# Optimization experiments

Measured on AMD Instinct MI355X. Metric: run time of the kernel, lower is better.

Reference implementation:

```python
import jax, jax.numpy as jnp
import numpy as np
from jax import lax

V = 100000       # vocab_size / num_words
E = 300          # embedding_size (== num_units, required by compare stage)
M = 300          # num_units / mem_dim
NC = 3           # num_classes
L = 128          # leaves per tree -> N = 2L-1 nodes
N = 2 * L - 1


def build_tree(num_leaves):
    # balanced binary tree, postorder node numbering (children before parent)
    left, right = [], []
    def rec(lo, hi):
        if hi - lo == 1:
            left.append(-1); right.append(-1)
            return len(left) - 1
        mid = (lo + hi) // 2
        l = rec(lo, mid)
        r = rec(mid, hi)
        left.append(l); right.append(r)
        return len(left) - 1
    rec(0, num_leaves)
    return np.asarray(left, np.int32), np.asarray(right, np.int32)


def setup_inputs() -> dict:
    key = jax.random.key(0)
    ks = jax.random.split(key, 20)
    l1, r1 = build_tree(L)
    l2, r2 = build_tree(L)
    s = 0.1  # param scale (stands in for orthogonal init)
    inp = {
        "sent1": jax.random.randint(ks[0], (N,), 0, V),
        "sent2": jax.random.randint(ks[1], (N,), 0, V),
        "left1": jnp.asarray(l1), "right1": jnp.asarray(r1),
        "left2": jnp.asarray(l2), "right2": jnp.asarray(r2),
        "emb": jax.random.normal(ks[2], (V, E), jnp.float32),
        # composer x-projections, gate order: [cx, ix, fx, ox]
        "Wx_i": jax.random.normal(ks[3], (4, M, E), jnp.float32) * s,
        "bx_i": jnp.zeros((4, M), jnp.float32),
        # composer h-projections, gate order: [u, i, lf, rf, o]
        "Wl_i": jax.random.normal(ks[4], (5, M, M), jnp.float32) * s,
        "Wr_i": jax.random.normal(ks[5], (5, M, M), jnp.float32) * s,
        "Wx_c": jax.random.normal(ks[6], (4, M, M), jnp.float32) * s,
        "bx_c": jnp.zeros((4, M), jnp.float32),
        "Wl_c": jax.random.normal(ks[7], (5, M, M), jnp.float32) * s,
        "Wr_c": jax.random.normal(ks[8], (5, M, M), jnp.float32) * s,
        "Wc": jax.random.normal(ks[9], (M, 4 * M), jnp.float32) * 0.01,
        "bc": jnp.zeros((M,), jnp.float32),
        "Wa1": jax.random.normal(ks[10], (M, 4 * M), jnp.float32) * 0.01,
        "ba1": jnp.zeros((M,), jnp.float32),
        "Wa2": jax.random.normal(ks[11], (NC, M), jnp.float32) * 0.01,
        "ba2": jnp.zeros((NC,), jnp.float32),
    }
    return inp


def tree_lstm(xg, left, right, Wl, Wr):
    # xg: [N, 4, M] precomputed x-gate terms (cx, ix, fx, ox)
    # Wl/Wr: [5, M, M] hidden-state gate weights (u, i, lf, rf, o)
    n, _, m = xg.shape
    zero = jnp.zeros((m,), xg.dtype)

    def step(carry, t):
        C, H = carry
        i, l, r = t
        lc = jnp.where(l >= 0, C[jnp.maximum(l, 0)], zero)
        lh = jnp.where(l >= 0, H[jnp.maximum(l, 0)], zero)
        rc = jnp.where(r >= 0, C[jnp.maximum(r, 0)], zero)
        rh = jnp.where(r >= 0, H[jnp.maximum(r, 0)], zero)
        gl = jnp.einsum('gmd,d->gm', Wl, lh)  # [5, M]
        gr = jnp.einsum('gmd,d->gm', Wr, rh)
        x = xg[i]  # [4, M]
        u  = jnp.tanh(x[0] + gl[0] + gr[0])
        ig = jax.nn.sigmoid(x[1] + gl[1] + gr[1])
        lf = jax.nn.sigmoid(x[2] + gl[2] + gr[2])  # fx shared for both forgets (as in source)
        rf = jax.nn.sigmoid(x[2] + gl[3] + gr[3])
        c = ig * u + lf * lc + rf * rc
        o = jax.nn.sigmoid(x[3] + gl[4] + gr[4])
        h = o * jnp.tanh(c)
        return (C.at[i].set(c), H.at[i].set(h)), None

    init = (jnp.zeros((n, m), xg.dtype), jnp.zeros((n, m), xg.dtype))
    (_, H), _ = lax.scan(step, init, (jnp.arange(n), left, right))
    return H  # [N, M] all node hidden states in postorder


def reference(sent1, sent2, left1, right1, left2, right2, emb,
              Wx_i, bx_i, Wl_i, Wr_i, Wx_c, bx_c, Wl_c, Wr_c,
              Wc, bc, Wa1, ba1, Wa2, ba2):
    pad = emb.shape[0] - 1  # num_words - 1

    def encode(sent, left, right):
        # leaves embed their token; internal nodes embed PAD (PAD=True path)
        tok = jnp.where(left < 0, sent, pad)
        x = emb[tok]                                        # [N, E]
        xg = jnp.einsum('nd,gmd->ngm', x, Wx_i) + bx_i      # [N, 4, M]
        return tree_lstm(xg, left, right, Wl_i, Wr_i)

    s1 = encode(sent1, left1, right1)  # [N1, M]
    s2 = encode(sent2, left2, right2)  # [N2, M]

    raw = s1 @ s2.T                                         # [N1, N2]
    beta = jax.nn.softmax(raw, axis=1) @ s2                 # aligned to s1
    alpha = jax.nn.softmax(raw.T, axis=1) @ s1              # aligned to s2

    def compare(s, a, left, right):
        feat = jnp.concatenate([s, a, s - a, s * a], axis=-1)  # [N, 4M]
        h = jax.nn.relu(feat @ Wc.T + bc)                      # [N, M]
        xg = jnp.einsum('nd,gmd->ngm', h, Wx_c) + bx_c
        return tree_lstm(xg, left, right, Wl_c, Wr_c)

    v1 = compare(s1, beta, left1, right1)
    v2 = compare(s2, alpha, left2, right2)

    agg = jnp.concatenate([v1.mean(0), v1.max(0), v2.mean(0), v2.max(0)])  # [4M]
    hidden = jax.nn.relu(agg @ Wa1.T + ba1)
    logits = hidden @ Wa2.T + ba2
    return logits[None, :]  # [1, num_classes]
```

## Files before the change

kernel.cpp:

```cpp
#include <hip/hip_runtime.h>
#include <math.h>

#define NN 255
#define MM 300
#define TC 510
#define NBLK 300
#define CHUNK 16
#define HTLD 512

__device__ __forceinline__ float sigm(float x) { return 1.0f / (1.0f + expf(-x)); }

__device__ __forceinline__ float aload(const float* p) {
  return __hip_atomic_load(p, __ATOMIC_RELAXED, __HIP_MEMORY_SCOPE_AGENT);
}
__device__ __forceinline__ void astore(float* p, float v) {
  __hip_atomic_store(p, v, __ATOMIC_RELAXED, __HIP_MEMORY_SCOPE_AGENT);
}

__device__ __forceinline__ void leaf_gate(const float* __restrict__ xgp, int m, float& c, float& h) {
  float x0 = xgp[m], x1 = xgp[300 + m], x3 = xgp[900 + m];
  float u  = tanhf(x0);
  float ig = sigm(x1);
  c = ig * u;
  h = sigm(x3) * tanhf(c);
}

__device__ __forceinline__ void gsync(unsigned* flags, unsigned phase) {
  asm volatile("s_waitcnt vmcnt(0)" ::: "memory");
  __syncthreads();
  unsigned* gate = flags + NBLK;
  if (blockIdx.x == 0) {
    if (threadIdx.x < 64) {
      for (;;) {
        unsigned mn = phase;
        for (int i = 1 + (int)threadIdx.x; i < NBLK; i += 64)
          mn = min(mn, __hip_atomic_load(&flags[i], __ATOMIC_RELAXED, __HIP_MEMORY_SCOPE_AGENT));
        if (__all(mn >= phase)) break;
        __builtin_amdgcn_s_sleep(2);
      }
      if (threadIdx.x == 0)
        __hip_atomic_store(gate, phase, __ATOMIC_RELAXED, __HIP_MEMORY_SCOPE_AGENT);
    }
  } else {
    if (threadIdx.x == 0) {
      __hip_atomic_store(&flags[blockIdx.x], phase, __ATOMIC_RELAXED, __HIP_MEMORY_SCOPE_AGENT);
      while (__hip_atomic_load(gate, __ATOMIC_RELAXED, __HIP_MEMORY_SCOPE_AGENT) < phase)
        __builtin_amdgcn_s_sleep(2);
    }
  }
  __syncthreads();
}

__global__ __launch_bounds__(512) void k_setup(const int* __restrict__ l1, const int* __restrict__ r1,
                                               const int* __restrict__ l2, const int* __restrict__ r2,
                                               int4* __restrict__ lists2, int* __restrict__ cnt)
{
  __shared__ int lv[TC];
  __shared__ int cs[16];
  int t = threadIdx.x;
  if (t < TC) lv[t] = 0;
  if (t < 16) cs[t] = 0;
  __syncthreads();
  for (int it = 0; it < 12; ++it) {
    int nv = 0;
    if (t < TC) {
      int tr = t >= NN;
      int i  = t - tr * NN;
      const int* L = tr ? l2 : l1;
      const int* R = tr ? r2 : r1;
      int l = L[i], r = R[i];
      nv = (l < 0) ? 0 : 1 + max(lv[tr * NN + l], lv[tr * NN + r]);
    }
    __syncthreads();
    if (t < TC) lv[t] = nv;
    __syncthreads();
  }
  if (t < TC) {
    int tr = t >= NN;
    int i  = t - tr * NN;
    int v  = min(lv[t], 15);
    int pos = atomicAdd(&cs[v], 1);
    int l = (tr ? l2 : l1)[i], r = (tr ? r2 : r1)[i];
    lists2[v * 256 + pos] = make_int4(tr * NN + i, tr * NN + max(l, 0), tr * NN + max(r, 0), 0);
  }
  __syncthreads();
  if (t < 16) cnt[t] = cs[t];
}

__global__ __launch_bounds__(256, 2) void k_tree(
    const int* __restrict__ l1, const int* __restrict__ l2,
    const float* __restrict__ Wl, const float* __restrict__ Wr,
    const float* __restrict__ xg,
    float* __restrict__ H, float* __restrict__ C, float* __restrict__ HT,
    const int4* __restrict__ lists2, const int* __restrict__ cnt,
    unsigned* __restrict__ bar)
{
  __shared__ float Hs[CHUNK][2][320];
  __shared__ float Cs[CHUNK][4][2];
  __shared__ float Xs[CHUNK][4][4];
  __shared__ int4 nfo[288];
  __shared__ int lvoff[9];

  const int tid  = threadIdx.x;
  const int lane = tid & 63;
  const int team = tid >> 6;
  const int mblk = blockIdx.x % 75;
  const int grp  = blockIdx.x / 75;
  const int m    = mblk * 4 + team;

  float wl[5][5], wr[5][5];
  #pragma unroll
  for (int g = 0; g < 5; ++g) {
    #pragma unroll
    for (int j = 0; j < 5; ++j) {
      int d = j * 64 + lane;
      size_t o = ((size_t)g * 300 + m) * 300 + d;
      wl[g][j] = (d < 300) ? Wl[o] : 0.f;
      wr[g][j] = (d < 300) ? Wr[o] : 0.f;
    }
  }

  if (tid == 0) { int o = 0; for (int lv = 1; lv <= 7; ++lv) { lvoff[lv] = o; o += cnt[lv]; } }
  __syncthreads();
  for (int lv = 1; lv <= 7; ++lv)
    for (int i = tid; i < cnt[lv]; i += 256)
      nfo[lvoff[lv] + i] = lists2[lv * 256 + i];

  for (int e = blockIdx.x * 256 + tid; e < TC * 300; e += 256 * NBLK) {
    int gi = e / 300;
    int mm = e - gi * 300;
    int tr = gi >= NN;
    int node = gi - tr * NN;
    if ((tr ? l2 : l1)[node] < 0) {
      float c, h;
      leaf_gate(xg + (size_t)gi * 1200, mm, c, h);
      astore(&C[(size_t)gi * 300 + mm], c);
      astore(&H[(size_t)gi * 300 + mm], h);
      astore(&HT[(size_t)mm * HTLD + gi], h);
    }
  }
  gsync(bar, 1);

  for (int lv = 1; lv <= 7; ++lv) {
    int nodes = cnt[lv];
    int npg = (nodes + 3) >> 2;
    int n0 = grp * npg;
    int n1 = min(nodes, n0 + npg);
    for (int nb = n0; nb < n1; nb += CHUNK) {
      int nch = min(CHUNK, n1 - nb);
      int base = lvoff[lv] + nb;
      __syncthreads();

      #pragma unroll
      for (int p = 0; p < 2; ++p) {
        int niA = team + p * 8;
        int niB = niA + 4;
        bool vA = niA < nch, vB = niB < nch;
        int4 na = vA ? nfo[base + niA] : make_int4(0, 0, 0, 0);
        int4 nb4 = vB ? nfo[base + niB] : make_int4(0, 0, 0, 0);
        float bA0, bA1, bA2, bA3, bA4, bA5, bA6, bA7, bA8, bA9;
        float bB0, bB1, bB2, bB3, bB4, bB5, bB6, bB7, bB8, bB9;
        #define LD(side_ptr, d, ok) ((ok) ? aload(&H[(size_t)(side_ptr) * 300 + (d)]) : 0.f)
        {
          int d0 = lane, d1 = 64 + lane, d2 = 128 + lane, d3 = 192 + lane, d4 = 256 + lane;
          bool i4 = d4 < 300;
          bA0 = LD(na.y, d0, vA); bA1 = LD(na.y, d1, vA); bA2 = LD(na.y, d2, vA);
          bA3 = LD(na.y, d3, vA); bA4 = LD(na.y, d4, vA && i4);
          bA5 = LD(na.z, d0, vA); bA6 = LD(na.z, d1, vA); bA7 = LD(na.z, d2, vA);
          bA8 = LD(na.z, d3, vA); bA9 = LD(na.z, d4, vA && i4);
          bB0 = LD(nb4.y, d0, vB); bB1 = LD(nb4.y, d1, vB); bB2 = LD(nb4.y, d2, vB);
          bB3 = LD(nb4.y, d3, vB); bB4 = LD(nb4.y, d4, vB && i4);
          bB5 = LD(nb4.z, d0, vB); bB6 = LD(nb4.z, d1, vB); bB7 = LD(nb4.z, d2, vB);
          bB8 = LD(nb4.z, d3, vB); bB9 = LD(nb4.z, d4, vB && i4);
          if (vA) {
            Hs[niA][0][d0] = bA0; Hs[niA][0][d1] = bA1; Hs[niA][0][d2] = bA2;
            Hs[niA][0][d3] = bA3; Hs[niA][0][d4] = bA4;
            Hs[niA][1][d0] = bA5; Hs[niA][1][d1] = bA6; Hs[niA][1][d2] = bA7;
            Hs[niA][1][d3] = bA8; Hs[niA][1][d4] = bA9;
          }
          if (vB) {
            Hs[niB][0][d0] = bB0; Hs[niB][0][d1] = bB1; Hs[niB][0][d2] = bB2;
            Hs[niB][0][d3] = bB3; Hs[niB][0][d4] = bB4;
            Hs[niB][1][d0] = bB5; Hs[niB][1][d1] = bB6; Hs[niB][1][d2] = bB7;
            Hs[niB][1][d3] = bB8; Hs[niB][1][d4] = bB9;
          }
        }
        #undef LD
      }
      if (tid < 128) {
        int ni = tid >> 3, tm = (tid >> 1) & 3, side = tid & 1;
        if (ni < nch) {
          int4 nn = nfo[base + ni];
          int child = side ? nn.z : nn.y;
          Cs[ni][tm][side] = aload(&C[(size_t)child * 300 + mblk * 4 + tm]);
        }
      }
      {
        int ni = tid >> 4, tm = (tid >> 2) & 3, g = tid & 3;
        if (ni < nch) {
          int4 nn = nfo[base + ni];
          Xs[ni][tm][g] = xg[(size_t)nn.x * 1200 + g * 300 + mblk * 4 + tm];
        }
      }
      __syncthreads();

      #pragma unroll 2
      for (int ni = 0; ni < nch; ++ni) {
        float p0 = 0.f, p1 = 0.f, p2 = 0.f, p3 = 0.f, p4 = 0.f;
        #pragma unroll
        for (int j = 0; j < 5; ++j) {
          float hl = Hs[ni][0][j * 64 + lane];
          float hr = Hs[ni][1][j * 64 + lane];
          p0 += wl[0][j] * hl + wr[0][j] * hr;
          p1 += wl[1][j] * hl + wr[1][j] * hr;
          p2 += wl[2][j] * hl + wr[2][j] * hr;
          p3 += wl[3][j] * hl + wr[3][j] * hr;
          p4 += wl[4][j] * hl + wr[4][j] * hr;
        }
        #pragma unroll
        for (int off = 32; off; off >>= 1) {
          p0 += __shfl_xor(p0, off);
          p1 += __shfl_xor(p1, off);
          p2 += __shfl_xor(p2, off);
          p3 += __shfl_xor(p3, off);
          p4 += __shfl_xor(p4, off);
        }
        if (lane == 0) {
          int4 nn = nfo[base + ni];
          int gi = nn.x;
          float lc = Cs[ni][team][0], rc = Cs[ni][team][1];
          float u  = tanhf(Xs[ni][team][0] + p0);
          float ig = sigm (Xs[ni][team][1] + p1);
          float lf = sigm (Xs[ni][team][2] + p2);
          float rf = sigm (Xs[ni][team][2] + p3);
          float o  = sigm (Xs[ni][team][3] + p4);
          float cc = ig * u + lf * lc + rf * rc;
          float hv = o * tanhf(cc);
          astore(&C[(size_t)gi * 300 + m], cc);
          astore(&H[(size_t)gi * 300 + m], hv);
          astore(&HT[(size_t)m * HTLD + gi], hv);
        }
      }
    }
    if (lv < 7) gsync(bar, 1 + lv);
  }
}

__global__ __launch_bounds__(256) void k_xg(const int* __restrict__ sent1, const int* __restrict__ sent2,
                                            const int* __restrict__ l1, const int* __restrict__ l2,
                                            const float* __restrict__ emb, int pad,
                                            const float* __restrict__ W, const float* __restrict__ bias,
                                            const float* __restrict__ hsrc, float* __restrict__ out)
{
  __shared__ float Z[8][300];
  int tx = threadIdx.x, ty = threadIdx.y;
  int t = ty * 64 + tx;
  int colbase = blockIdx.y * 8;
  for (int c = 0; c < 8; ++c) {
    int gcol = colbase + c;
    if (gcol < TC) {
      if (hsrc) {
        for (int k = t; k < 300; k += 256) Z[c][k] = hsrc[(size_t)gcol * 300 + k];
      } else {
        int tr = gcol >= NN;
        int node = gcol - tr * NN;
        const int* L = tr ? l2 : l1;
        const int* S = tr ? sent2 : sent1;
        int tok = (L[node] < 0) ? S[node] : pad;
        const float* e = emb + (size_t)tok * 300;
        for (int k = t; k < 300; k += 256) Z[c][k] = e[k];
      }
    } else {
      for (int k = t; k < 300; k += 256) Z[c][k] = 0.f;
    }
  }
  __syncthreads();
  int r = blockIdx.x * 64 + tx;
  if (r < 1200) {
    float a0 = 0.f, a1 = 0.f;
    const float* wp = W + (size_t)r * 300;
    for (int k = 0; k < 300; k += 4) {
      float4 wv = *(const float4*)(wp + k);
      float4 z0 = *(const float4*)(&Z[ty][k]);
      float4 z1 = *(const float4*)(&Z[ty + 4][k]);
      a0 += wv.x*z0.x + wv.y*z0.y + wv.z*z0.z + wv.w*z0.w;
      a1 += wv.x*z1.x + wv.y*z1.y + wv.z*z1.z + wv.w*z1.w;
    }
    float b = bias[r];
    int g0 = colbase + ty, g1 = colbase + ty + 4;
    if (g0 < TC) out[(size_t)g0 * 1200 + r] = a0 + b;
    if (g1 < TC) out[(size_t)g1 * 1200 + r] = a1 + b;
  }
}

__global__ __launch_bounds__(256) void k_attn(const float* __restrict__ H, const float* __restrict__ HT,
                                              float* __restrict__ ab)
{
  __shared__ float q[300];
  __shared__ float pr[NN];
  __shared__ float red[256];
  int b = blockIdx.x, t = threadIdx.x;
  int dir = b >= NN;
  int i = b - dir * NN;
  const float* Ss = H + (dir ? NN * 300 : 0);
  const float* So = H + (dir ? 0 : NN * 300);
  int oppb = dir ? 0 : NN;
  for (int k = t; k < 300; k += 256) q[k] = Ss[(size_t)i * 300 + k];
  __syncthreads();
  float v = -1e30f;
  if (t < NN) {
    float a = 0.f;
    const float* hp = HT + oppb + t;
    #pragma unroll 4
    for (int k = 0; k < 300; ++k) a += q[k] * hp[(size_t)k * HTLD];
    pr[t] = a;
    v = a;
  }
  red[t] = v;
  __syncthreads();
  for (int s = 128; s > 0; s >>= 1) { if (t < s) red[t] = fmaxf(red[t], red[t + s]); __syncthreads(); }
  float mx = red[0];
  __syncthreads();
  float e = 0.f;
  if (t < NN) { e = expf(pr[t] - mx); pr[t] = e; }
  red[t] = e;
  __syncthreads();
  for (int s = 128; s > 0; s >>= 1) { if (t < s) red[t] += red[t + s]; __syncthreads(); }
  float inv = 1.0f / red[0];
  __syncthreads();
  for (int m = t; m < 300; m += 256) {
    float a = 0.f;
    for (int j = 0; j < NN; ++j) a += pr[j] * So[(size_t)j * 300 + m];
    ab[(size_t)b * 300 + m] = a * inv;
  }
}

__global__ __launch_bounds__(256) void k_hcmp(const float* __restrict__ Henc, const float* __restrict__ ab,
                                              const float* __restrict__ Wc, const float* __restrict__ bc,
                                              float* __restrict__ hc)
{
  __shared__ float Z[8][1200];
  int tx = threadIdx.x, ty = threadIdx.y;
  int t = ty * 64 + tx;
  int colbase = blockIdx.y * 8;
  for (int c = 0; c < 8; ++c) {
    int gcol = colbase + c;
    if (gcol < TC) {
      const float* sp = Henc + (size_t)gcol * 300;
      const float* ap = ab + (size_t)gcol * 300;
      for (int k = t; k < 1200; k += 256) {
        int sel = k >= 900 ? 3 : (k >= 600 ? 2 : (k >= 300 ? 1 : 0));
        int kk = k - sel * 300;
        float s = sp[kk], a = ap[kk];
        Z[c][k] = sel == 0 ? s : sel == 1 ? a : sel == 2 ? (s - a) : (s * a);
      }
    } else {
      for (int k = t; k < 1200; k += 256) Z[c][k] = 0.f;
    }
  }
  __syncthreads();
  int r = blockIdx.x * 64 + tx;
  if (r < 300) {
    float a0 = 0.f, a1 = 0.f;
    const float* wp = Wc + (size_t)r * 1200;
    for (int k = 0; k < 1200; k += 4) {
      float4 wv = *(const float4*)(wp + k);
      float4 z0 = *(const float4*)(&Z[ty][k]);
      float4 z1 = *(const float4*)(&Z[ty + 4][k]);
      a0 += wv.x*z0.x + wv.y*z0.y + wv.z*z0.z + wv.w*z0.w;
      a1 += wv.x*z1.x + wv.y*z1.y + wv.z*z1.z + wv.w*z1.w;
    }
    float b = bc[r];
    int g0 = colbase + ty, g1 = colbase + ty + 4;
    if (g0 < TC) hc[(size_t)g0 * 300 + r] = fmaxf(a0 + b, 0.f);
    if (g1 < TC) hc[(size_t)g1 * 300 + r] = fmaxf(a1 + b, 0.f);
  }
}

__global__ __launch_bounds__(512) void k_head(const float* __restrict__ HTc,
                                              const float* __restrict__ Wa1, const float* __restrict__ ba1,
                                              const float* __restrict__ Wa2, const float* __restrict__ ba2,
                                              float* __restrict__ out)
{
  __shared__ float a_s[1200];
  __shared__ float hid[300];
  int t = threadIdx.x;
  for (int idx = t; idx < 600; idx += 512) {
    int tr = idx >= 300;
    int m = idx - tr * 300;
    const float* p = HTc + (size_t)m * HTLD + tr * NN;
    float s = 0.f, mx = -1e30f;
    for (int n = 0; n < NN; ++n) { float v = p[n]; s += v; mx = fmaxf(mx, v); }
    a_s[tr * 600 + m] = s / 255.0f;
    a_s[tr * 600 + 300 + m] = mx;
  }
  __syncthreads();
  for (int h = t; h < 300; h += 512) {
    float acc = ba1[h];
    const float* wp = Wa1 + (size_t)h * 1200;
    for (int k = 0; k < 1200; k += 4) {
      float4 wv = *(const float4*)(wp + k);
      float4 av = *(const float4*)(&a_s[k]);
      acc += wv.x*av.x + wv.y*av.y + wv.z*av.z + wv.w*av.w;
    }
    hid[h] = fmaxf(acc, 0.f);
  }
  __syncthreads();
  if (t < 192) {
    int c = t >> 6, lane = t & 63;
    float a = 0.f;
    for (int k = lane; k < 300; k += 64) a += Wa2[c * 300 + k] * hid[k];
    for (int off = 32; off > 0; off >>= 1) a += __shfl_down(a, off);
    if (lane == 0) out[c] = a + ba2[c];
  }
}

extern "C" void kernel_launch(void* const* d_in, const int* in_sizes, int n_in,
                              void* d_out, int out_size, void* d_ws, size_t ws_size,
                              hipStream_t stream)
{
  const int*   sent1 = (const int*)d_in[0];
  const int*   sent2 = (const int*)d_in[1];
  const int*   l1    = (const int*)d_in[2];
  const int*   r1    = (const int*)d_in[3];
  const int*   l2    = (const int*)d_in[4];
  const int*   r2    = (const int*)d_in[5];
  const float* emb   = (const float*)d_in[6];
  const float* Wx_i  = (const float*)d_in[7];
  const float* bx_i  = (const float*)d_in[8];
  const float* Wl_i  = (const float*)d_in[9];
  const float* Wr_i  = (const float*)d_in[10];
  const float* Wx_c  = (const float*)d_in[11];
  const float* bx_c  = (const float*)d_in[12];
  const float* Wl_c  = (const float*)d_in[13];
  const float* Wr_c  = (const float*)d_in[14];
  const float* Wc    = (const float*)d_in[15];
  const float* bc    = (const float*)d_in[16];
  const float* Wa1   = (const float*)d_in[17];
  const float* ba1   = (const float*)d_in[18];
  const float* Wa2   = (const float*)d_in[19];
  const float* ba2   = (const float*)d_in[20];
  int V = in_sizes[6] / 300;
  int pad = V - 1;

  char* w = (char*)d_ws;
  unsigned* bar1 = (unsigned*)w;
  unsigned* bar2 = (unsigned*)(w + 2048);
  int* cnt     = (int*)(w + 4096);
  int4* lists2 = (int4*)(w + 4160);
  float* xg   = (float*)(w + 4160 + 65536);
  float* Henc = xg + 612000;
  float* Hcmp = Henc + 153000;
  float* C    = Hcmp + 153000;
  float* ab   = C + 153000;
  float* hc   = ab + 153000;
  float* HTe  = hc + 153000;
  float* HTc  = HTe + 153600;

  hipMemsetAsync((void*)bar1, 0, 4096, stream);
  k_setup<<<1, 512, 0, stream>>>(l1, r1, l2, r2, lists2, cnt);

  dim3 blk(64, 4);

  k_xg<<<dim3(19, 64), blk, 0, stream>>>(sent1, sent2, l1, l2, emb, pad, Wx_i, bx_i, nullptr, xg);
  {
    void* args[] = {(void*)&l1, (void*)&l2,
                    (void*)&Wl_i, (void*)&Wr_i, (void*)&xg,
                    (void*)&Henc, (void*)&C, (void*)&HTe,
                    (void*)&lists2, (void*)&cnt, (void*)&bar1};
    hipLaunchCooperativeKernel((void*)k_tree, dim3(NBLK), dim3(256), args, 0, stream);
  }

  k_attn<<<TC, 256, 0, stream>>>(Henc, HTe, ab);

  k_hcmp<<<dim3(5, 64), blk, 0, stream>>>(Henc, ab, Wc, bc, hc);
  k_xg<<<dim3(19, 64), blk, 0, stream>>>(sent1, sent2, l1, l2, emb, pad, Wx_c, bx_c, hc, xg);
  {
    void* args[] = {(void*)&l1, (void*)&l2,
                    (void*)&Wl_c, (void*)&Wr_c, (void*)&xg,
                    (void*)&Hcmp, (void*)&C, (void*)&HTc,
                    (void*)&lists2, (void*)&cnt, (void*)&bar2};
    hipLaunchCooperativeKernel((void*)k_tree, dim3(NBLK), dim3(256), args, 0, stream);
  }

  k_head<<<1, 512, 0, stream>>>(HTc, Wa1, ba1, Wa2, ba2, (float*)d_out);
}
```

Measured before the change: 503.8 us.

## Double tree-LSTM cooperative grid to 600 blocks and use fence-based barrier

New measurement: 796.8 us. 58.2% more time.

```diff
diff --git a/kernel.cpp b/kernel.cpp
--- a/kernel.cpp
+++ b/kernel.cpp
@@ -2,53 +2,47 @@
 #include <math.h>
 
 #define NN 255
-#define MM 300
 #define TC 510
-#define NBLK 300
-#define CHUNK 16
 #define HTLD 512
 
-__device__ __forceinline__ float sigm(float x) { return 1.0f / (1.0f + expf(-x)); }
-
-__device__ __forceinline__ float aload(const float* p) {
-  return __hip_atomic_load(p, __ATOMIC_RELAXED, __HIP_MEMORY_SCOPE_AGENT);
-}
-__device__ __forceinline__ void astore(float* p, float v) {
-  __hip_atomic_store(p, v, __ATOMIC_RELAXED, __HIP_MEMORY_SCOPE_AGENT);
-}
-
-__device__ __forceinline__ void leaf_gate(const float* __restrict__ xgp, int m, float& c, float& h) {
-  float x0 = xgp[m], x1 = xgp[300 + m], x3 = xgp[900 + m];
-  float u  = tanhf(x0);
-  float ig = sigm(x1);
+typedef unsigned int uint32;
+
+__device__ __forceinline__ float sigm(float x){ return 1.f/(1.f+expf(-x)); }
+
+__device__ __forceinline__ uint32 aloadu(const uint32* p){ return __hip_atomic_load(p, __ATOMIC_RELAXED, __HIP_MEMORY_SCOPE_AGENT); }
+__device__ __forceinline__ void astoreu(uint32* p, uint32 v){ __hip_atomic_store(p, v, __ATOMIC_RELAXED, __HIP_MEMORY_SCOPE_AGENT); }
+
+__device__ __forceinline__ void leaf_gate(const float* __restrict__ xgp, int m, float& c, float& h){
+  float x0 = xgp[m], x1 = xgp[300+m], x3 = xgp[900+m];
+  float u = tanhf(x0), ig = sigm(x1);
   c = ig * u;
   h = sigm(x3) * tanhf(c);
 }
 
-__device__ __forceinline__ void gsync(unsigned* flags, unsigned phase) {
-  asm volatile("s_waitcnt vmcnt(0)" ::: "memory");
-  __syncthreads();
-  unsigned* gate = flags + NBLK;
-  if (blockIdx.x == 0) {
-    if (threadIdx.x < 64) {
-      for (;;) {
-        unsigned mn = phase;
-        for (int i = 1 + (int)threadIdx.x; i < NBLK; i += 64)
-          mn = min(mn, __hip_atomic_load(&flags[i], __ATOMIC_RELAXED, __HIP_MEMORY_SCOPE_AGENT));
+template<int NB>
+__device__ __forceinline__ void gsyncf(uint32* flags, uint32 phase){
+  __builtin_amdgcn_fence(__ATOMIC_RELEASE, "agent");
+  __syncthreads();
+  uint32* gate = flags + NB;
+  if (blockIdx.x == 0){
+    if (threadIdx.x < 64){
+      for(;;){
+        uint32 mn = phase;
+        for (int i = 1 + (int)threadIdx.x; i < NB; i += 64)
+          mn = min(mn, aloadu(&flags[i]));
         if (__all(mn >= phase)) break;
         __builtin_amdgcn_s_sleep(2);
       }
-      if (threadIdx.x == 0)
-        __hip_atomic_store(gate, phase, __ATOMIC_RELAXED, __HIP_MEMORY_SCOPE_AGENT);
+      if (threadIdx.x == 0) astoreu(gate, phase);
     }
   } else {
-    if (threadIdx.x == 0) {
-      __hip_atomic_store(&flags[blockIdx.x], phase, __ATOMIC_RELAXED, __HIP_MEMORY_SCOPE_AGENT);
-      while (__hip_atomic_load(gate, __ATOMIC_RELAXED, __HIP_MEMORY_SCOPE_AGENT) < phase)
-        __builtin_amdgcn_s_sleep(2);
-    }
-  }
-  __syncthreads();
+    if (threadIdx.x == 0){
+      astoreu(&flags[blockIdx.x], phase);
+      while (aloadu(gate) < phase) __builtin_amdgcn_s_sleep(2);
+    }
+  }
+  __syncthreads();
+  __builtin_amdgcn_fence(__ATOMIC_ACQUIRE, "agent");
 }
 
 __global__ __launch_bounds__(512) void k_setup(const int* __restrict__ l1, const int* __restrict__ r1,
@@ -61,11 +55,10 @@
   if (t < TC) lv[t] = 0;
   if (t < 16) cs[t] = 0;
   __syncthreads();
-  for (int it = 0; it < 12; ++it) {
+  for (int it = 0; it < 12; ++it){
     int nv = 0;
-    if (t < TC) {
-      int tr = t >= NN;
-      int i  = t - tr * NN;
+    if (t < TC){
+      int tr = t >= NN, i = t - tr * NN;
       const int* L = tr ? l2 : l1;
       const int* R = tr ? r2 : r1;
       int l = L[i], r = R[i];
@@ -75,10 +68,9 @@
     if (t < TC) lv[t] = nv;
     __syncthreads();
   }
-  if (t < TC) {
-    int tr = t >= NN;
-    int i  = t - tr * NN;
-    int v  = min(lv[t], 15);
+  if (t < TC){
+    int tr = t >= NN, i = t - tr * NN;
+    int v = min(lv[t], 15);
     int pos = atomicAdd(&cs[v], 1);
     int l = (tr ? l2 : l1)[i], r = (tr ? r2 : r1)[i];
     lists2[v * 256 + pos] = make_int4(tr * NN + i, tr * NN + max(l, 0), tr * NN + max(r, 0), 0);
@@ -87,128 +79,107 @@
   if (t < 16) cnt[t] = cs[t];
 }
 
-__global__ __launch_bounds__(256, 2) void k_tree(
+template<int NB, int NG>
+__global__ __launch_bounds__(256, 3) void k_tree(
     const int* __restrict__ l1, const int* __restrict__ l2,
     const float* __restrict__ Wl, const float* __restrict__ Wr,
     const float* __restrict__ xg,
     float* __restrict__ H, float* __restrict__ C, float* __restrict__ HT,
     const int4* __restrict__ lists2, const int* __restrict__ cnt,
-    unsigned* __restrict__ bar)
-{
-  __shared__ float Hs[CHUNK][2][320];
-  __shared__ float Cs[CHUNK][4][2];
-  __shared__ float Xs[CHUNK][4][4];
+    uint32* __restrict__ bar)
+{
+  __shared__ float Hs[16][2][320];
+  __shared__ float Cs[16][4][2];
+  __shared__ float Xs[16][4][4];
   __shared__ int4 nfo[288];
   __shared__ int lvoff[9];
 
-  const int tid  = threadIdx.x;
-  const int lane = tid & 63;
-  const int team = tid >> 6;
-  const int mblk = blockIdx.x % 75;
-  const int grp  = blockIdx.x / 75;
-  const int m    = mblk * 4 + team;
+  const int tid = threadIdx.x;
+  const int lane = tid & 63, team = tid >> 6;
+  const int mblk = blockIdx.x % 75, grp = blockIdx.x / 75;
+  const int m = mblk * 4 + team;
 
   float wl[5][5], wr[5][5];
   #pragma unroll
-  for (int g = 0; g < 5; ++g) {
+  for (int g = 0; g < 5; ++g)
     #pragma unroll
-    for (int j = 0; j < 5; ++j) {
+    for (int j = 0; j < 5; ++j){
       int d = j * 64 + lane;
       size_t o = ((size_t)g * 300 + m) * 300 + d;
       wl[g][j] = (d < 300) ? Wl[o] : 0.f;
       wr[g][j] = (d < 300) ? Wr[o] : 0.f;
     }
-  }
-
-  if (tid == 0) { int o = 0; for (int lv = 1; lv <= 7; ++lv) { lvoff[lv] = o; o += cnt[lv]; } }
+
+  if (tid == 0){ int o = 0; for (int lv = 1; lv <= 7; ++lv){ lvoff[lv] = o; o += cnt[lv]; } }
   __syncthreads();
   for (int lv = 1; lv <= 7; ++lv)
     for (int i = tid; i < cnt[lv]; i += 256)
       nfo[lvoff[lv] + i] = lists2[lv * 256 + i];
 
-  for (int e = blockIdx.x * 256 + tid; e < TC * 300; e += 256 * NBLK) {
-    int gi = e / 300;
-    int mm = e - gi * 300;
-    int tr = gi >= NN;
-    int node = gi - tr * NN;
-    if ((tr ? l2 : l1)[node] < 0) {
-      float c, h;
-      leaf_gate(xg + (size_t)gi * 1200, mm, c, h);
-      astore(&C[(size_t)gi * 300 + mm], c);
-      astore(&H[(size_t)gi * 300 + mm], h);
-      astore(&HT[(size_t)mm * HTLD + gi], h);
-    }
-  }
-  gsync(bar, 1);
-
-  for (int lv = 1; lv <= 7; ++lv) {
+  for (int e = blockIdx.x * 256 + tid; e < TC * 300; e += 256 * NB){
+    int gi = e / 300, mm = e - gi * 300;
+    int tr = gi >= NN, node = gi - tr * NN;
+    if ((tr ? l2 : l1)[node] < 0){
+      float c, h; leaf_gate(xg + (size_t)gi * 1200, mm, c, h);
+      C[(size_t)gi * 300 + mm] = c;
+      H[(size_t)gi * 300 + mm] = h;
+      HT[(size_t)mm * HTLD + gi] = h;
+    }
+  }
+  gsyncf<NB>(bar, 1);
+
+  for (int lv = 1; lv <= 7; ++lv){
     int nodes = cnt[lv];
-    int npg = (nodes + 3) >> 2;
-    int n0 = grp * npg;
-    int n1 = min(nodes, n0 + npg);
-    for (int nb = n0; nb < n1; nb += CHUNK) {
-      int nch = min(CHUNK, n1 - nb);
-      int base = lvoff[lv] + nb;
+    int npg = (nodes + NG - 1) / NG;
+    int n0 = grp * npg, n1 = min(nodes, n0 + npg);
+    for (int nb0 = n0; nb0 < n1; nb0 += 16){
+      int nch = min(16, n1 - nb0);
+      int base = lvoff[lv] + nb0;
       __syncthreads();
-
       #pragma unroll
-      for (int p = 0; p < 2; ++p) {
-        int niA = team + p * 8;
-        int niB = niA + 4;
+      for (int p = 0; p < 2; ++p){
+        int niA = team + p * 8, niB = niA + 4;
         bool vA = niA < nch, vB = niB < nch;
         int4 na = vA ? nfo[base + niA] : make_int4(0, 0, 0, 0);
         int4 nb4 = vB ? nfo[base + niB] : make_int4(0, 0, 0, 0);
-        float bA0, bA1, bA2, bA3, bA4, bA5, bA6, bA7, bA8, bA9;
-        float bB0, bB1, bB2, bB3, bB4, bB5, bB6, bB7, bB8, bB9;
-        #define LD(side_ptr, d, ok) ((ok) ? aload(&H[(size_t)(side_ptr) * 300 + (d)]) : 0.f)
-        {
-          int d0 = lane, d1 = 64 + lane, d2 = 128 + lane, d3 = 192 + lane, d4 = 256 + lane;
-          bool i4 = d4 < 300;
-          bA0 = LD(na.y, d0, vA); bA1 = LD(na.y, d1, vA); bA2 = LD(na.y, d2, vA);
-          bA3 = LD(na.y, d3, vA); bA4 = LD(na.y, d4, vA && i4);
-          bA5 = LD(na.z, d0, vA); bA6 = LD(na.z, d1, vA); bA7 = LD(na.z, d2, vA);
-          bA8 = LD(na.z, d3, vA); bA9 = LD(na.z, d4, vA && i4);
-          bB0 = LD(nb4.y, d0, vB); bB1 = LD(nb4.y, d1, vB); bB2 = LD(nb4.y, d2, vB);
-          bB3 = LD(nb4.y, d3, vB); bB4 = LD(nb4.y, d4, vB && i4);
-          bB5 = LD(nb4.z, d0, vB); bB6 = LD(nb4.z, d1, vB); bB7 = LD(nb4.z, d2, vB);
-          bB8 = LD(nb4.z, d3, vB); bB9 = LD(nb4.z, d4, vB && i4);
-          if (vA) {
-            Hs[niA][0][d0] = bA0; Hs[niA][0][d1] = bA1; Hs[niA][0][d2] = bA2;
-            Hs[niA][0][d3] = bA3; Hs[niA][0][d4] = bA4;
-            Hs[niA][1][d0] = bA5; Hs[niA][1][d1] = bA6; Hs[niA][1][d2] = bA7;
-            Hs[niA][1][d3] = bA8; Hs[niA][1][d4] = bA9;
-          }
-          if (vB) {
-            Hs[niB][0][d0] = bB0; Hs[niB][0][d1] = bB1; Hs[niB][0][d2] = bB2;
-            Hs[niB][0][d3] = bB3; Hs[niB][0][d4] = bB4;
-            Hs[niB][1][d0] = bB5; Hs[niB][1][d1] = bB6; Hs[niB][1][d2] = bB7;
-            Hs[niB][1][d3] = bB8; Hs[niB][1][d4] = bB9;
-          }
-        }
-        #undef LD
-      }
-      if (tid < 128) {
+        int d0 = lane, d1 = 64 + lane, d2 = 128 + lane, d3 = 192 + lane, d4 = 256 + lane;
+        bool i4 = d4 < 300;
+        #define LDH(ci, dd, ok) ((ok) ? H[(size_t)(ci) * 300 + (dd)] : 0.f)
+        float a0=LDH(na.y,d0,vA), a1=LDH(na.y,d1,vA), a2=LDH(na.y,d2,vA), a3=LDH(na.y,d3,vA), a4=LDH(na.y,d4,vA&&i4);
+        float a5=LDH(na.z,d0,vA), a6=LDH(na.z,d1,vA), a7=LDH(na.z,d2,vA), a8=LDH(na.z,d3,vA), a9=LDH(na.z,d4,vA&&i4);
+        float c0=LDH(nb4.y,d0,vB), c1=LDH(nb4.y,d1,vB), c2=LDH(nb4.y,d2,vB), c3=LDH(nb4.y,d3,vB), c4=LDH(nb4.y,d4,vB&&i4);
+        float c5=LDH(nb4.z,d0,vB), c6=LDH(nb4.z,d1,vB), c7=LDH(nb4.z,d2,vB), c8=LDH(nb4.z,d3,vB), c9=LDH(nb4.z,d4,vB&&i4);
+        #undef LDH
+        if (vA){
+          Hs[niA][0][d0]=a0; Hs[niA][0][d1]=a1; Hs[niA][0][d2]=a2; Hs[niA][0][d3]=a3; Hs[niA][0][d4]=a4;
+          Hs[niA][1][d0]=a5; Hs[niA][1][d1]=a6; Hs[niA][1][d2]=a7; Hs[niA][1][d3]=a8; Hs[niA][1][d4]=a9;
+        }
+        if (vB){
+          Hs[niB][0][d0]=c0; Hs[niB][0][d1]=c1; Hs[niB][0][d2]=c2; Hs[niB][0][d3]=c3; Hs[niB][0][d4]=c4;
+          Hs[niB][1][d0]=c5; Hs[niB][1][d1]=c6; Hs[niB][1][d2]=c7; Hs[niB][1][d3]=c8; Hs[niB][1][d4]=c9;
+        }
+      }
+      if (tid < 128){
         int ni = tid >> 3, tm = (tid >> 1) & 3, side = tid & 1;
-        if (ni < nch) {
+        if (ni < nch){
           int4 nn = nfo[base + ni];
           int child = side ? nn.z : nn.y;
-          Cs[ni][tm][side] = aload(&C[(size_t)child * 300 + mblk * 4 + tm]);
+          Cs[ni][tm][side] = C[(size_t)child * 300 + mblk * 4 + tm];
         }
       }
       {
         int ni = tid >> 4, tm = (tid >> 2) & 3, g = tid & 3;
-        if (ni < nch) {
+        if (ni < nch){
           int4 nn = nfo[base + ni];
           Xs[ni][tm][g] = xg[(size_t)nn.x * 1200 + g * 300 + mblk * 4 + tm];
         }
       }
       __syncthreads();
-
       #pragma unroll 2
-      for (int ni = 0; ni < nch; ++ni) {
+      for (int ni = 0; ni < nch; ++ni){
         float p0 = 0.f, p1 = 0.f, p2 = 0.f, p3 = 0.f, p4 = 0.f;
         #pragma unroll
-        for (int j = 0; j < 5; ++j) {
+        for (int j = 0; j < 5; ++j){
           float hl = Hs[ni][0][j * 64 + lane];
           float hr = Hs[ni][1][j * 64 + lane];
           p0 += wl[0][j] * hl + wr[0][j] * hr;
@@ -218,14 +189,11 @@
           p4 += wl[4][j] * hl + wr[4][j] * hr;
         }
         #pragma unroll
-        for (int off = 32; off; off >>= 1) {
-          p0 += __shfl_xor(p0, off);
-          p1 += __shfl_xor(p1, off);
-          p2 += __shfl_xor(p2, off);
-          p3 += __shfl_xor(p3, off);
-          p4 += __shfl_xor(p4, off);
-        }
-        if (lane == 0) {
+        for (int off = 32; off; off >>= 1){
+          p0 += __shfl_xor(p0, off); p1 += __shfl_xor(p1, off); p2 += __shfl_xor(p2, off);
+          p3 += __shfl_xor(p3, off); p4 += __shfl_xor(p4, off);
+        }
+        if (lane == 0){
           int4 nn = nfo[base + ni];
           int gi = nn.x;
           float lc = Cs[ni][team][0], rc = Cs[ni][team][1];
@@ -236,13 +204,13 @@
           float o  = sigm (Xs[ni][team][3] + p4);
           float cc = ig * u + lf * lc + rf * rc;
           float hv = o * tanhf(cc);
-          astore(&C[(size_t)gi * 300 + m], cc);
-          astore(&H[(size_t)gi * 300 + m], hv);
-          astore(&HT[(size_t)m * HTLD + gi], hv);
-        }
-      }
-    }
-    if (lv < 7) gsync(bar, 1 + lv);
+          C[(size_t)gi * 300 + m] = cc;
+          H[(size_t)gi * 300 + m] = hv;
+          HT[(size_t)m * HTLD + gi] = hv;
+        }
+      }
+    }
+    if (lv < 7) gsyncf<NB>(bar, 1 + lv);
   }
 }
 
@@ -256,17 +224,14 @@
   int tx = threadIdx.x, ty = threadIdx.y;
   int t = ty * 64 + tx;
   int colbase = blockIdx.y * 8;
-  for (int c = 0; c < 8; ++c) {
+  for (int c = 0; c < 8; ++c){
     int gcol = colbase + c;
-    if (gcol < TC) {
-      if (hsrc) {
+    if (gcol < TC){
+      if (hsrc){
         for (int k = t; k < 300; k += 256) Z[c][k] = hsrc[(size_t)gcol * 300 + k];
       } else {
-        int tr = gcol >= NN;
-        int node = gcol - tr * NN;
-        const int* L = tr ? l2 : l1;
-        const int* S = tr ? sent2 : sent1;
-        int tok = (L[node] < 0) ? S[node] : pad;
+        int tr = gcol >= NN, node = gcol - tr * NN;
+        int tok = ((tr ? l2 : l1)[node] < 0) ? (tr ? sent2 : sent1)[node] : pad;
         const float* e = emb + (size_t)tok * 300;
         for (int k = t; k < 300; k += 256) Z[c][k] = e[k];
       }
@@ -276,10 +241,10 @@
   }
   __syncthreads();
   int r = blockIdx.x * 64 + tx;
-  if (r < 1200) {
+  if (r < 1200){
     float a0 = 0.f, a1 = 0.f;
     const float* wp = W + (size_t)r * 300;
-    for (int k = 0; k < 300; k += 4) {
+    for (int k = 0; k < 300; k += 4){
       float4 wv = *(const float4*)(wp + k);
       float4 z0 = *(const float4*)(&Z[ty][k]);
       float4 z1 = *(const float4*)(&Z[ty + 4][k]);
@@ -300,35 +265,29 @@
   __shared__ float pr[NN];
   __shared__ float red[256];
   int b = blockIdx.x, t = threadIdx.x;
-  int dir = b >= NN;
-  int i = b - dir * NN;
+  int dir = b >= NN, i = b - dir * NN;
   const float* Ss = H + (dir ? NN * 300 : 0);
   const float* So = H + (dir ? 0 : NN * 300);
   int oppb = dir ? 0 : NN;
   for (int k = t; k < 300; k += 256) q[k] = Ss[(size_t)i * 300 + k];
   __syncthreads();
   float v = -1e30f;
-  if (t < NN) {
+  if (t < NN){
     float a = 0.f;
     const float* hp = HT + oppb + t;
     #pragma unroll 4
     for (int k = 0; k < 300; ++k) a += q[k] * hp[(size_t)k * HTLD];
-    pr[t] = a;
-    v = a;
-  }
-  red[t] = v;
-  __syncthreads();
-  for (int s = 128; s > 0; s >>= 1) { if (t < s) red[t] = fmaxf(red[t], red[t + s]); __syncthreads(); }
-  float mx = red[0];
-  __syncthreads();
+    pr[t] = a; v = a;
+  }
+  red[t] = v; __syncthreads();
+  for (int s = 128; s; s >>= 1){ if (t < s) red[t] = fmaxf(red[t], red[t + s]); __syncthreads(); }
+  float mx = red[0]; __syncthreads();
   float e = 0.f;
-  if (t < NN) { e = expf(pr[t] - mx); pr[t] = e; }
-  red[t] = e;
-  __syncthreads();
-  for (int s = 128; s > 0; s >>= 1) { if (t < s) red[t] += red[t + s]; __syncthreads(); }
-  float inv = 1.0f / red[0];
-  __syncthreads();
-  for (int m = t; m < 300; m += 256) {
+  if (t < NN){ e = expf(pr[t] - mx); pr[t] = e; }
+  red[t] = e; __syncthreads();
+  for (int s = 128; s; s >>= 1){ if (t < s) red[t] += red[t + s]; __syncthreads(); }
+  float inv = 1.f / red[0]; __syncthreads();
+  for (int m = t; m < 300; m += 256){
     float a = 0.f;
     for (int j = 0; j < NN; ++j) a += pr[j] * So[(size_t)j * 300 + m];
     ab[(size_t)b * 300 + m] = a * inv;
@@ -343,12 +302,12 @@
   int tx = threadIdx.x, ty = threadIdx.y;
   int t = ty * 64 + tx;
   int colbase = blockIdx.y * 8;
-  for (int c = 0; c < 8; ++c) {
+  for (int c = 0; c < 8; ++c){
     int gcol = colbase + c;
-    if (gcol < TC) {
+    if (gcol < TC){
       const float* sp = Henc + (size_t)gcol * 300;
       const float* ap = ab + (size_t)gcol * 300;
-      for (int k = t; k < 1200; k += 256) {
+      for (int k = t; k < 1200; k += 256){
         int sel = k >= 900 ? 3 : (k >= 600 ? 2 : (k >= 300 ? 1 : 0));
         int kk = k - sel * 300;
         float s = sp[kk], a = ap[kk];
@@ -360,10 +319,10 @@
   }
   __syncthreads();
   int r = blockIdx.x * 64 + tx;
-  if (r < 300) {
+  if (r < 300){
     float a0 = 0.f, a1 = 0.f;
     const float* wp = Wc + (size_t)r * 1200;
-    for (int k = 0; k < 1200; k += 4) {
+    for (int k = 0; k < 1200; k += 4){
       float4 wv = *(const float4*)(wp + k);
       float4 z0 = *(const float4*)(&Z[ty][k]);
       float4 z1 = *(const float4*)(&Z[ty + 4][k]);
@@ -385,20 +344,20 @@
   __shared__ float a_s[1200];
   __shared__ float hid[300];
   int t = threadIdx.x;
-  for (int idx = t; idx < 600; idx += 512) {
+  for (int idx = t; idx < 600; idx += 512){
     int tr = idx >= 300;
     int m = idx - tr * 300;
     const float* p = HTc + (size_t)m * HTLD + tr * NN;
     float s = 0.f, mx = -1e30f;
-    for (int n = 0; n < NN; ++n) { float v = p[n]; s += v; mx = fmaxf(mx, v); }
+    for (int n = 0; n < NN; ++n){ float v = p[n]; s += v; mx = fmaxf(mx, v); }
     a_s[tr * 600 + m] = s / 255.0f;
     a_s[tr * 600 + 300 + m] = mx;
   }
   __syncthreads();
-  for (int h = t; h < 300; h += 512) {
+  for (int h = t; h < 300; h += 512){
     float acc = ba1[h];
     const float* wp = Wa1 + (size_t)h * 1200;
-    for (int k = 0; k < 1200; k += 4) {
+    for (int k = 0; k < 1200; k += 4){
       float4 wv = *(const float4*)(wp + k);
       float4 av = *(const float4*)(&a_s[k]);
       acc += wv.x*av.x + wv.y*av.y + wv.z*av.z + wv.w*av.w;
@@ -406,11 +365,11 @@
     hid[h] = fmaxf(acc, 0.f);
   }
   __syncthreads();
-  if (t < 192) {
+  if (t < 192){
     int c = t >> 6, lane = t & 63;
     float a = 0.f;
     for (int k = lane; k < 300; k += 64) a += Wa2[c * 300 + k] * hid[k];
-    for (int off = 32; off > 0; off >>= 1) a += __shfl_down(a, off);
+    for (int off = 32; off; off >>= 1) a += __shfl_down(a, off);
     if (lane == 0) out[c] = a + ba2[c];
   }
 }
@@ -434,8 +393,8 @@
   const float* bx_c  = (const float*)d_in[12];
   const float* Wl_c  = (const float*)d_in[13];
   const float* Wr_c  = (const float*)d_in[14];
-  const float* Wc    = (const float*)d_in[15];
-  const float* bc    = (const float*)d_in[16];
+  const float* Wcm   = (const float*)d_in[15];
+  const float* bcm   = (const float*)d_in[16];
   const float* Wa1   = (const float*)d_in[17];
   const float* ba1   = (const float*)d_in[18];
   const float* Wa2   = (const float*)d_in[19];
@@ -444,11 +403,11 @@
   int pad = V - 1;
 
   char* w = (char*)d_ws;
-  unsigned* bar1 = (unsigned*)w;
-  unsigned* bar2 = (unsigned*)(w + 2048);
-  int* cnt     = (int*)(w + 4096);
-  int4* lists2 = (int4*)(w + 4160);
-  float* xg   = (float*)(w + 4160 + 65536);
+  uint32* bar1   = (uint32*)w;
+  uint32* bar2   = (uint32*)(w + 4096);
+  int*    cnt    = (int*)(w + 8192);
+  int4*   lists2 = (int4*)(w + 8256);
+  float* xg   = (float*)(w + 8256 + 65536);
   float* Henc = xg + 612000;
   float* Hcmp = Henc + 153000;
   float* C    = Hcmp + 153000;
@@ -456,32 +415,36 @@
   float* hc   = ab + 153000;
   float* HTe  = hc + 153000;
   float* HTc  = HTe + 153600;
-
-  hipMemsetAsync((void*)bar1, 0, 4096, stream);
+  float* outp = (float*)d_out;
+
+  hipMemsetAsync(bar1, 0, 8192, stream);
+
+  int nb6 = 0, nCU = 0;
+  hipError_t eq = hipOccupancyMaxActiveBlocksPerMultiprocessor(&nb6, reinterpret_cast<const void*>(&k_tree<600, 8>), 256, 0);
+  hipError_t ec = hipDeviceGetAttribute(&nCU, hipDeviceAttributeMultiprocessorCount, 0);
+  bool ok600 = (eq == hipSuccess) && (ec == hipSuccess) && (nb6 * nCU >= 600);
+
   k_setup<<<1, 512, 0, stream>>>(l1, r1, l2, r2, lists2, cnt);
-
   dim3 blk(64, 4);
 
   k_xg<<<dim3(19, 64), blk, 0, stream>>>(sent1, sent2, l1, l2, emb, pad, Wx_i, bx_i, nullptr, xg);
   {
-    void* args[] = {(void*)&l1, (void*)&l2,
-                    (void*)&Wl_i, (void*)&Wr_i, (void*)&xg,
-                    (void*)&Henc, (void*)&C, (void*)&HTe,
-                    (void*)&lists2, (void*)&cnt, (void*)&bar1};
-    hipLaunchCooperativeKernel((void*)k_tree, dim3(NBLK), dim3(256), args, 0, stream);
+    void* args[] = {(void*)&l1, (void*)&l2, (void*)&Wl_i, (void*)&Wr_i, (void*)&xg,
+                    (void*)&Henc, (void*)&C, (void*)&HTe, (void*)&lists2, (void*)&cnt, (void*)&bar1};
+    if (ok600) hipLaunchCooperativeKernel((void*)&k_tree<600, 8>, dim3(600), dim3(256), args, 0, stream);
+    else       hipLaunchCooperativeKernel((void*)&k_tree<300, 4>, dim3(300), dim3(256), args, 0, stream);
   }
 
   k_attn<<<TC, 256, 0, stream>>>(Henc, HTe, ab);
 
-  k_hcmp<<<dim3(5, 64), blk, 0, stream>>>(Henc, ab, Wc, bc, hc);
+  k_hcmp<<<dim3(5, 64), blk, 0, stream>>>(Henc, ab, Wcm, bcm, hc);
   k_xg<<<dim3(19, 64), blk, 0, stream>>>(sent1, sent2, l1, l2, emb, pad, Wx_c, bx_c, hc, xg);
   {
-    void* args[] = {(void*)&l1, (void*)&l2,
-                    (void*)&Wl_c, (void*)&Wr_c, (void*)&xg,
-                    (void*)&Hcmp, (void*)&C, (void*)&HTc,
-                    (void*)&lists2, (void*)&cnt, (void*)&bar2};
-    hipLaunchCooperativeKernel((void*)k_tree, dim3(NBLK), dim3(256), args, 0, stream);
-  }
-
-  k_head<<<1, 512, 0, stream>>>(HTc, Wa1, ba1, Wa2, ba2, (float*)d_out);
-}
+    void* args[] = {(void*)&l1, (void*)&l2, (void*)&Wl_c, (void*)&Wr_c, (void*)&xg,
+                    (void*)&Hcmp, (void*)&C, (void*)&HTc, (void*)&lists2, (void*)&cnt, (void*)&bar2};
+    if (ok600) hipLaunchCooperativeKernel((void*)&k_tree<600, 8>, dim3(600), dim3(256), args, 0, stream);
+    else       hipLaunchCooperativeKernel((void*)&k_tree<300, 4>, dim3(300), dim3(256), args, 0, stream);
+  }
+
+  k_head<<<1, 512, 0, stream>>>(HTc, Wa1, ba1, Wa2, ba2, outp);
+}
```
